# Performance work log

Hardware: AMD Instinct MI355X
Metric: run time of the kernel (lower is better)

Reference implementation:

```python
import jax, jax.numpy as jnp
import numpy as np

DIM = 1024
HEADS = 16
DIM_HEAD = 64
INNER = HEADS * DIM_HEAD  # 1024
SCALE = DIM_HEAD ** -0.5


def layernorm(x, gamma, beta, eps=1e-5):
    mu = jnp.mean(x, axis=-1, keepdims=True)
    var = jnp.var(x, axis=-1, keepdims=True)
    return (x - mu) * jax.lax.rsqrt(var + eps) * gamma + beta


def setup_inputs() -> dict:
    key = jax.random.key(0)
    ks = jax.random.split(key, 6)
    x = jax.random.normal(ks[0], (2, 2048, DIM), dtype=jnp.float32)
    # params (stored [in, out]; torch Linear does x @ W.T with W [out, in])
    w_q = jax.random.normal(ks[1], (DIM, INNER), dtype=jnp.float32) * (DIM ** -0.5)
    w_kv = jax.random.normal(ks[2], (DIM, 2 * INNER), dtype=jnp.float32) * (DIM ** -0.5)
    w_out = jax.random.normal(ks[3], (INNER, DIM), dtype=jnp.float32) * (INNER ** -0.5)
    b_out = jnp.zeros((DIM,), dtype=jnp.float32)
    gamma = jnp.ones((DIM,), dtype=jnp.float32)
    beta = jnp.zeros((DIM,), dtype=jnp.float32)
    return {"x": x, "w_q": w_q, "w_kv": w_kv, "w_out": w_out, "b_out": b_out,
            "gamma": gamma, "beta": beta}


def reference(x, w_q, w_kv, w_out, b_out, gamma, beta):
    b, n, _ = x.shape
    xn = layernorm(x, gamma, beta)
    q = xn @ w_q                           # [b, n, inner]
    kv = xn @ w_kv                         # [b, n, 2*inner]
    k, v = jnp.split(kv, 2, axis=-1)
    def split_heads(t):
        return t.reshape(b, n, HEADS, DIM_HEAD).transpose(0, 2, 1, 3)  # b h n d
    q, k, v = split_heads(q), split_heads(k), split_heads(v)
    dots = jnp.einsum('bhid,bhjd->bhij', q, k) * SCALE   # [b, h, n, n]
    attn = jax.nn.softmax(dots, axis=-1)
    out = jnp.einsum('bhij,bhjd->bhid', attn, v)          # [b, h, n, d]
    out = out.transpose(0, 2, 1, 3).reshape(b, n, INNER)  # b n (h d)
    return out @ w_out + b_out
```

## Files before the change

### kernel.cpp

```cpp
#include <hip/hip_runtime.h>

typedef unsigned short u16;
typedef u16   u16x8 __attribute__((ext_vector_type(8)));
typedef __bf16 bf16x8 __attribute__((ext_vector_type(8)));
typedef float f32x4 __attribute__((ext_vector_type(4)));
typedef float f32x2 __attribute__((ext_vector_type(2)));
typedef _Float16 f16x4 __attribute__((ext_vector_type(4)));
typedef _Float16 f16x8 __attribute__((ext_vector_type(8)));
typedef unsigned u32x2 __attribute__((ext_vector_type(2)));

__device__ __forceinline__ u16 f2b(float f){ __bf16 h=(__bf16)f; return __builtin_bit_cast(u16,h); }

__device__ __forceinline__ f32x4 mfma16(u16x8 a, u16x8 b, f32x4 c){
  return __builtin_amdgcn_mfma_f32_16x16x32_bf16(
      __builtin_bit_cast(bf16x8,a), __builtin_bit_cast(bf16x8,b), c, 0,0,0);
}

__device__ __forceinline__ void gl2lds16(const u16* g, u16* l){
  __builtin_amdgcn_global_load_lds((const __attribute__((address_space(1))) void*)g,
                                   (__attribute__((address_space(3))) void*)l, 16, 0, 0);
}

__global__ __launch_bounds__(256) void ln_kernel(const float* __restrict__ x,
                                                 const float* __restrict__ gamma,
                                                 const float* __restrict__ beta,
                                                 u16* __restrict__ xn){
  const int row = blockIdx.x, t = threadIdx.x;
  const float4 v = ((const float4*)(x + (size_t)row*1024))[t];
  float s  = v.x+v.y+v.z+v.w;
  float sq = v.x*v.x+v.y*v.y+v.z*v.z+v.w*v.w;
  for (int m=1;m<64;m<<=1){ s += __shfl_xor(s,m); sq += __shfl_xor(sq,m); }
  __shared__ float red[8];
  const int w=t>>6, l=t&63;
  if(l==0){ red[w]=s; red[4+w]=sq; }
  __syncthreads();
  const float S  = red[0]+red[1]+red[2]+red[3];
  const float SQ = red[4]+red[5]+red[6]+red[7];
  const float mu = S*(1.f/1024.f);
  const float var= SQ*(1.f/1024.f)-mu*mu;
  const float rs = rsqrtf(var+1e-5f);
  const float4 g4=((const float4*)gamma)[t], b4=((const float4*)beta)[t];
  u16 o0=f2b((v.x-mu)*rs*g4.x+b4.x);
  u16 o1=f2b((v.y-mu)*rs*g4.y+b4.y);
  u16 o2=f2b((v.z-mu)*rs*g4.z+b4.z);
  u16 o3=f2b((v.w-mu)*rs*g4.w+b4.w);
  uint2 p; p.x=(unsigned)o0|((unsigned)o1<<16); p.y=(unsigned)o2|((unsigned)o3<<16);
  ((uint2*)(xn + (size_t)row*1024))[t]=p;
}

__global__ __launch_bounds__(256) void wtrans_all_kernel(const float* __restrict__ wq,
    const float* __restrict__ wkv, const float* __restrict__ wout,
    u16* __restrict__ wqkvt, u16* __restrict__ woutt){
  __shared__ float tile[64][65];
  const int bx=blockIdx.x, t=threadIdx.x;
  const float* in; u16* out; int C, cxx;
  if(bx<16){ in=wq;  out=wqkvt;           C=1024; cxx=bx; }
  else if(bx<48){ in=wkv; out=wqkvt+1024*1024; C=2048; cxx=bx-16; }
  else { in=wout; out=woutt;             C=1024; cxx=bx-48; }
  const int R=1024;
  const int c0=cxx*64, r0=blockIdx.y*64;
  {
    const int r=t>>2, cc=t&3;
    const float* gp = in + (size_t)(r0+r)*C + c0 + cc*16;
    #pragma unroll
    for(int i=0;i<4;i++){
      float4 f=((const float4*)gp)[i];
      tile[r][cc*16+i*4+0]=f.x; tile[r][cc*16+i*4+1]=f.y;
      tile[r][cc*16+i*4+2]=f.z; tile[r][cc*16+i*4+3]=f.w;
    }
  }
  __syncthreads();
  const int c=t>>2, rc=t&3;
  u16x8 a,b;
  #pragma unroll
  for(int i=0;i<8;i++) a[i]=f2b(tile[rc*16+i][c]);
  #pragma unroll
  for(int i=0;i<8;i++) b[i]=f2b(tile[rc*16+8+i][c]);
  u16* op = out + (size_t)(c0+c)*R + r0 + rc*16;
  *(u16x8*)op=a; *(u16x8*)(op+8)=b;
}

template<int MODE,int TM>
__global__ __launch_bounds__(256) void gemm_bt_kernel(const u16* __restrict__ A,
    const u16* __restrict__ Bt, u16* __restrict__ outQ, u16* __restrict__ outK,
    u16* __restrict__ outV, float* __restrict__ outF, const float* __restrict__ bias,
    float scale, int M, int N, int K){
  constexpr int MT = TM/32;
  __shared__ u16 As[TM*64];
  __shared__ u16 Bs[128*64];
  const int t=threadIdx.x, w=t>>6, l=t&63, qd=l>>4, ln=l&15;
  const int m0=blockIdx.y*TM, n0=blockIdx.x*128;
  const int wm=(w>>1)*(TM/2), wn=(w&1)*64;
  f32x4 acc[MT][4] = {};
  const int nK = K>>6;
  for(int kt=0; kt<nK; kt++){
    const int k0=kt*64;
    #pragma unroll
    for(int p=0;p<MT;p++){
      const int cid=p*256+t, r=cid>>3, pc=cid&7, g=pc^(r&7);
      gl2lds16(A + (size_t)(m0+r)*K + k0 + g*8, &As[(p*256 + (t&192))*8]);
    }
    #pragma unroll
    for(int p=0;p<4;p++){
      const int cid=p*256+t, r=cid>>3, pc=cid&7, g=pc^(r&7);
      gl2lds16(Bt + (size_t)(n0+r)*K + k0 + g*8, &Bs[(p*256 + (t&192))*8]);
    }
    __syncthreads();
    #pragma unroll
    for(int ks=0;ks<2;ks++){
      u16x8 af[MT], bf[4];
      #pragma unroll
      for(int mt=0;mt<MT;mt++){
        const int m=wm+mt*16+ln, kc=ks*4+qd, pcc=kc^(m&7);
        af[mt]=*(const u16x8*)&As[m*64 + pcc*8];
      }
      #pragma unroll
      for(int nt=0;nt<4;nt++){
        const int n=wn+nt*16+ln, kc=ks*4+qd, pcc=kc^(n&7);
        bf[nt]=*(const u16x8*)&Bs[n*64 + pcc*8];
      }
      #pragma unroll
      for(int mt=0;mt<MT;mt++)
        #pragma unroll
        for(int nt=0;nt<4;nt++)
          acc[mt][nt]=mfma16(af[mt],bf[nt],acc[mt][nt]);
    }
    __syncthreads();
  }
  if(MODE==1){
    #pragma unroll
    for(int mt=0;mt<MT;mt++)
      #pragma unroll
      for(int rr=0;rr<4;rr++){
        const int row = m0+wm+mt*16+qd*4+rr;
        #pragma unroll
        for(int nt=0;nt<4;nt++){
          const int col = n0+wn+nt*16+ln;
          outF[(size_t)row*N+col]=acc[mt][nt][rr]+bias[col];
        }
      }
  } else if(n0<1024){
    #pragma unroll
    for(int mt=0;mt<MT;mt++)
      #pragma unroll
      for(int rr=0;rr<4;rr++){
        const int row = m0+wm+mt*16+qd*4+rr;
        #pragma unroll
        for(int nt=0;nt<4;nt++)
          outQ[(size_t)row*1024 + n0+wn+nt*16+ln]=f2b(acc[mt][nt][rr]*scale);
      }
  } else if(n0<2048){
    u16* kp = outK + (size_t)((m0>>11)*16 + ((n0-1024+wn)>>6))*131072;
    const int jb = (m0&2047) + wm;
    #pragma unroll
    for(int mt=0;mt<MT;mt++)
      #pragma unroll
      for(int rr=0;rr<4;rr++){
        const int j = jb + mt*16 + qd*4 + rr;
        #pragma unroll
        for(int nt=0;nt<4;nt++)
          kp[(size_t)j*64 + nt*16+ln]=f2b(acc[mt][nt][rr]);
      }
  } else {
    u16* vpp = outV + (size_t)((m0>>11)*16 + ((n0-2048+wn)>>6))*131072;
    const int jb = (m0&2047) + wm;
    #pragma unroll
    for(int mt=0;mt<MT;mt++){
      const int j = jb + mt*16 + qd*4;
      const int vbase = ((j>>5)*4 + ((j>>2)&3))*512 + ((j>>4)&1)*4;
      #pragma unroll
      for(int nt=0;nt<4;nt++){
        const auto lo=__builtin_amdgcn_cvt_pkrtz(acc[mt][nt][0],acc[mt][nt][1]);
        const auto hi=__builtin_amdgcn_cvt_pkrtz(acc[mt][nt][2],acc[mt][nt][3]);
        uint2 w2; w2.x=__builtin_bit_cast(unsigned,lo); w2.y=__builtin_bit_cast(unsigned,hi);
        *(uint2*)&vpp[vbase + (nt*16+ln)*8] = w2;
      }
    }
  }
}

__global__ __launch_bounds__(256,4) void attn_kernel(const u16* __restrict__ Q,
    const u16* __restrict__ Kp, const u16* __restrict__ Vp, u16* __restrict__ O){
  __shared__ u16 Ks[8192];
  __shared__ u16 Vs[8192];
  const int qt=blockIdx.x, h=blockIdx.y, bb=blockIdx.z;
  const int t=threadIdx.x, w=t>>6, l=t&63, qd=l>>4, ln=l&15;
  const int q0=qt*64;
  const size_t baseQ=(size_t)bb*2048*1024 + h*64;
  const size_t baseKV=(size_t)(bb*16+h)*131072;
  u16x8 qf[2];
  #pragma unroll
  for(int ks=0;ks<2;ks++)
    qf[ks] = *(const u16x8*)(Q + baseQ + (size_t)(q0+w*16+ln)*1024 + ks*32+qd*8);
  f32x2 l2={0.f,0.f};
  f32x4 o_acc[4]={};
  const f32x4 zf={0.f,0.f,0.f,0.f};

  for(int j0=0;j0<2048;j0+=128){
    __syncthreads();
    #pragma unroll
    for(int p=0;p<4;p++){
      const int r=(p*256+t)>>3, g=(t&7)^((t>>3)&7);
      gl2lds16(Kp + baseKV + (size_t)(j0+r)*64 + g*8, &Ks[(p*256+(t&192))*8]);
    }
    #pragma unroll
    for(int p=0;p<4;p++){
      gl2lds16(Vp + baseKV + (size_t)(j0>>5)*2048 + (size_t)(p*256+t)*8,
               &Vs[(p*256+(t&192))*8]);
    }
    __syncthreads();

    #pragma unroll
    for(int jh=0;jh<2;jh++){
      f32x4 s[4];
      #pragma unroll
      for(int ks=0;ks<2;ks++){
        u16x8 kf[4];
        #pragma unroll
        for(int j4=0;j4<4;j4++){
          const int row=(jh*4+j4)*16+ln;
          kf[j4]=*(const u16x8*)&Ks[row*64 + (((ks*4+qd)^(ln&7))*8)];
        }
        #pragma unroll
        for(int j4=0;j4<4;j4++)
          s[j4] = ks? mfma16(kf[j4],qf[1],s[j4]) : mfma16(kf[j4],qf[0],zf);
      }
      #pragma unroll
      for(int al=0;al<2;al++){
        const int a=jh*2+al;
        f16x8 vf2[4];
        #pragma unroll
        for(int dt=0;dt<4;dt++)
          vf2[dt]=*(const f16x8*)&Vs[((a*4+qd)*64 + dt*16+ln)*8];
        #pragma unroll
        for(int tt=0;tt<2;tt++){
          const int j4l=al*2+tt;
          const float p0=exp2f(s[j4l][0]), p1=exp2f(s[j4l][1]);
          const float p2=exp2f(s[j4l][2]), p3=exp2f(s[j4l][3]);
          f32x2 pa; pa.x=p0; pa.y=p1;
          f32x2 pb; pb.x=p2; pb.y=p3;
          l2+=pa+pb;
          const auto lo=__builtin_amdgcn_cvt_pkrtz(p0,p1);
          const auto hi=__builtin_amdgcn_cvt_pkrtz(p2,p3);
          u32x2 pu; pu.x=__builtin_bit_cast(unsigned,lo); pu.y=__builtin_bit_cast(unsigned,hi);
          const f16x4 pf=__builtin_bit_cast(f16x4,pu);
          #pragma unroll
          for(int dt=0;dt<4;dt++){
            const f16x4 vf=tt? __builtin_shufflevector(vf2[dt],vf2[dt],4,5,6,7)
                             : __builtin_shufflevector(vf2[dt],vf2[dt],0,1,2,3);
            o_acc[dt]=__builtin_amdgcn_mfma_f32_16x16x16f16(pf,vf,o_acc[dt],0,0,0);
          }
        }
      }
    }
  }

  float li=l2.x+l2.y;
  li+=__shfl_xor(li,16);
  li+=__shfl_xor(li,32);
  const float linv=1.f/li;
  #pragma unroll
  for(int rr=0;rr<4;rr++){
    const float lr=__shfl(linv,qd*4+rr);
    const int row=q0+w*16+qd*4+rr;
    #pragma unroll
    for(int dt=0;dt<4;dt++)
      O[baseQ + (size_t)row*1024 + dt*16+ln]=f2b(o_acc[dt][rr]*lr);
  }
}

extern "C" void kernel_launch(void* const* d_in, const int* in_sizes, int n_in,
                              void* d_out, int out_size, void* d_ws, size_t ws_size,
                              hipStream_t stream) {
  const float* x     = (const float*)d_in[0];
  const float* w_q   = (const float*)d_in[1];
  const float* w_kv  = (const float*)d_in[2];
  const float* w_out = (const float*)d_in[3];
  const float* b_out = (const float*)d_in[4];
  const float* gamma = (const float*)d_in[5];
  const float* beta  = (const float*)d_in[6];
  float* out = (float*)d_out;

  char* ws=(char*)d_ws;
  size_t off=0;
  u16* xn    =(u16*)(ws+off); off += (size_t)4096*1024*2;
  u16* wqkvt =(u16*)(ws+off); off += (size_t)3072*1024*2;
  u16* woutt =(u16*)(ws+off); off += (size_t)1024*1024*2;
  u16* qb    =(u16*)(ws+off); off += (size_t)4096*1024*2;
  u16* kpb   =(u16*)(ws+off); off += (size_t)4096*1024*2;
  u16* vpb   =(u16*)(ws+off); off += (size_t)4096*1024*2;
  u16* ob    =(u16*)(ws+off); off += (size_t)4096*1024*2;

  ln_kernel<<<4096,256,0,stream>>>(x,gamma,beta,xn);
  wtrans_all_kernel<<<dim3(64,16),256,0,stream>>>(w_q,w_kv,w_out,wqkvt,woutt);

  const float SCALE_Q = 0.125f*1.4426950408889634f;
  gemm_bt_kernel<2,128><<<dim3(24,32),256,0,stream>>>(xn,wqkvt,qb,kpb,vpb,nullptr,nullptr,SCALE_Q,4096,3072,1024);
  attn_kernel<<<dim3(32,16,2),256,0,stream>>>(qb,kpb,vpb,ob);
  gemm_bt_kernel<1,64><<<dim3(8,64),256,0,stream>>>(ob,woutt,nullptr,nullptr,nullptr,out,b_out,1.f,4096,1024,1024);
}
```

Baseline: 197.3 us.

## Split attention key range across warp pairs with 32-row query tiles and LDS reduction

Each warp now owns 32 query rows (two 16-row tiles) and half of the 128-key block, instead of 16 rows over all keys. Every K fragment loaded from LDS is reused for two query tiles, and each warp reads only half of the V fragments, which cuts LDS read traffic per MFMA. At the end, the two warps sharing a query half combine their partial outputs and row sums through shared memory. The cost is more accumulator registers, an extra reduction step and two barriers at the end.

```diff
diff --git a/kernel.cpp b/kernel.cpp
--- a/kernel.cpp
+++ b/kernel.cpp
@@ -181,19 +181,23 @@
 
 __global__ __launch_bounds__(256,4) void attn_kernel(const u16* __restrict__ Q,
     const u16* __restrict__ Kp, const u16* __restrict__ Vp, u16* __restrict__ O){
-  __shared__ u16 Ks[8192];
-  __shared__ u16 Vs[8192];
+  __shared__ u16 lds[16384];
+  u16* Ks = lds;
+  u16* Vs = lds+8192;
   const int qt=blockIdx.x, h=blockIdx.y, bb=blockIdx.z;
   const int t=threadIdx.x, w=t>>6, l=t&63, qd=l>>4, ln=l&15;
+  const int ih=w&1, jh2=w>>1;
   const int q0=qt*64;
   const size_t baseQ=(size_t)bb*2048*1024 + h*64;
   const size_t baseKV=(size_t)(bb*16+h)*131072;
-  u16x8 qf[2];
+  u16x8 qf[2][2];
   #pragma unroll
-  for(int ks=0;ks<2;ks++)
-    qf[ks] = *(const u16x8*)(Q + baseQ + (size_t)(q0+w*16+ln)*1024 + ks*32+qd*8);
-  f32x2 l2={0.f,0.f};
-  f32x4 o_acc[4]={};
+  for(int it=0;it<2;it++)
+    #pragma unroll
+    for(int ks=0;ks<2;ks++)
+      qf[it][ks] = *(const u16x8*)(Q + baseQ + (size_t)(q0+ih*32+it*16+ln)*1024 + ks*32+qd*8);
+  f32x2 l2[2]={{0.f,0.f},{0.f,0.f}};
+  f32x4 o_acc[2][4]={};
   const f32x4 zf={0.f,0.f,0.f,0.f};
 
   for(int j0=0;j0<2048;j0+=128){
@@ -210,36 +214,38 @@
     }
     __syncthreads();
 
-    #pragma unroll
-    for(int jh=0;jh<2;jh++){
-      f32x4 s[4];
-      #pragma unroll
-      for(int ks=0;ks<2;ks++){
-        u16x8 kf[4];
-        #pragma unroll
-        for(int j4=0;j4<4;j4++){
-          const int row=(jh*4+j4)*16+ln;
-          kf[j4]=*(const u16x8*)&Ks[row*64 + (((ks*4+qd)^(ln&7))*8)];
-        }
-        #pragma unroll
-        for(int j4=0;j4<4;j4++)
-          s[j4] = ks? mfma16(kf[j4],qf[1],s[j4]) : mfma16(kf[j4],qf[0],zf);
-      }
-      #pragma unroll
-      for(int al=0;al<2;al++){
-        const int a=jh*2+al;
-        f16x8 vf2[4];
-        #pragma unroll
-        for(int dt=0;dt<4;dt++)
-          vf2[dt]=*(const f16x8*)&Vs[((a*4+qd)*64 + dt*16+ln)*8];
-        #pragma unroll
-        for(int tt=0;tt<2;tt++){
-          const int j4l=al*2+tt;
-          const float p0=exp2f(s[j4l][0]), p1=exp2f(s[j4l][1]);
-          const float p2=exp2f(s[j4l][2]), p3=exp2f(s[j4l][3]);
+    f32x4 s[2][4];
+    #pragma unroll
+    for(int ks=0;ks<2;ks++){
+      u16x8 kf[4];
+      #pragma unroll
+      for(int jt=0;jt<4;jt++){
+        const int row=jh2*64+jt*16+ln;
+        kf[jt]=*(const u16x8*)&Ks[row*64 + (((ks*4+qd)^(ln&7))*8)];
+      }
+      #pragma unroll
+      for(int jt=0;jt<4;jt++){
+        if(ks==0){ s[0][jt]=mfma16(kf[jt],qf[0][0],zf); s[1][jt]=mfma16(kf[jt],qf[1][0],zf); }
+        else     { s[0][jt]=mfma16(kf[jt],qf[0][1],s[0][jt]); s[1][jt]=mfma16(kf[jt],qf[1][1],s[1][jt]); }
+      }
+    }
+    #pragma unroll
+    for(int al=0;al<2;al++){
+      const int a=jh2*2+al;
+      f16x8 vf2[4];
+      #pragma unroll
+      for(int dt=0;dt<4;dt++)
+        vf2[dt]=*(const f16x8*)&Vs[((a*4+qd)*64 + dt*16+ln)*8];
+      #pragma unroll
+      for(int tt=0;tt<2;tt++){
+        const int jt=al*2+tt;
+        #pragma unroll
+        for(int it=0;it<2;it++){
+          const float p0=exp2f(s[it][jt][0]), p1=exp2f(s[it][jt][1]);
+          const float p2=exp2f(s[it][jt][2]), p3=exp2f(s[it][jt][3]);
           f32x2 pa; pa.x=p0; pa.y=p1;
           f32x2 pb; pb.x=p2; pb.y=p3;
-          l2+=pa+pb;
+          l2[it]+=pa+pb;
           const auto lo=__builtin_amdgcn_cvt_pkrtz(p0,p1);
           const auto hi=__builtin_amdgcn_cvt_pkrtz(p2,p3);
           u32x2 pu; pu.x=__builtin_bit_cast(unsigned,lo); pu.y=__builtin_bit_cast(unsigned,hi);
@@ -248,24 +254,48 @@
           for(int dt=0;dt<4;dt++){
             const f16x4 vf=tt? __builtin_shufflevector(vf2[dt],vf2[dt],4,5,6,7)
                              : __builtin_shufflevector(vf2[dt],vf2[dt],0,1,2,3);
-            o_acc[dt]=__builtin_amdgcn_mfma_f32_16x16x16f16(pf,vf,o_acc[dt],0,0,0);
+            o_acc[it][dt]=__builtin_amdgcn_mfma_f32_16x16x16f16(pf,vf,o_acc[it][dt],0,0,0);
           }
         }
       }
     }
   }
 
-  float li=l2.x+l2.y;
-  li+=__shfl_xor(li,16);
-  li+=__shfl_xor(li,32);
-  const float linv=1.f/li;
-  #pragma unroll
-  for(int rr=0;rr<4;rr++){
-    const float lr=__shfl(linv,qd*4+rr);
-    const int row=q0+w*16+qd*4+rr;
-    #pragma unroll
-    for(int dt=0;dt<4;dt++)
-      O[baseQ + (size_t)row*1024 + dt*16+ln]=f2b(o_acc[dt][rr]*lr);
+  __syncthreads();
+  float* cb=(float*)lds;
+  if(jh2==1){
+    const int base=(ih*64+l)*36;
+    #pragma unroll
+    for(int it=0;it<2;it++)
+      #pragma unroll
+      for(int dt=0;dt<4;dt++)
+        *(f32x4*)&cb[base+(it*4+dt)*4]=o_acc[it][dt];
+    cb[base+32]=l2[0].x+l2[0].y;
+    cb[base+33]=l2[1].x+l2[1].y;
+  }
+  __syncthreads();
+  if(jh2==0){
+    const int base=(ih*64+l)*36;
+    #pragma unroll
+    for(int it=0;it<2;it++)
+      #pragma unroll
+      for(int dt=0;dt<4;dt++)
+        o_acc[it][dt]+=*(const f32x4*)&cb[base+(it*4+dt)*4];
+    #pragma unroll
+    for(int it=0;it<2;it++){
+      float li=l2[it].x+l2[it].y + cb[base+32+it];
+      li+=__shfl_xor(li,16);
+      li+=__shfl_xor(li,32);
+      const float linv=1.f/li;
+      #pragma unroll
+      for(int rr=0;rr<4;rr++){
+        const float lr=__shfl(linv,qd*4+rr);
+        const int row=q0+ih*32+it*16+qd*4+rr;
+        #pragma unroll
+        for(int dt=0;dt<4;dt++)
+          O[baseQ + (size_t)row*1024 + dt*16+ln]=f2b(o_acc[it][dt][rr]*lr);
+      }
+    }
   }
 }
 
```

Result: slower. 205.0 us (+3.9%).
